# Kernel optimization log

Hardware: AMD Instinct MI355X
Metric: run time of the kernel (lower is better)

## Reference

```python
import jax, jax.numpy as jnp
import numpy as np

NUM_ITERATIONS = 5
DEPTH_L = 2
NUM_NODES = 8448
MAX_CHECK_NEIGHBORS = 10
BATCH = 1024


def setup_inputs() -> dict:
    key = jax.random.key(0)
    k1, k2, k3 = jax.random.split(key, 3)
    input_llr = jax.random.normal(k1, (BATCH, NUM_NODES), dtype=jnp.float32)
    w_ch = jnp.ones((NUM_NODES,), dtype=jnp.float32)
    w_res = jnp.ones((DEPTH_L, NUM_NODES), dtype=jnp.float32)
    check_index_tensor = jax.random.randint(k2, (NUM_NODES, MAX_CHECK_NEIGHBORS), 0, NUM_NODES, dtype=jnp.int32)
    var_index_tensor = jax.random.randint(k3, (NUM_NODES, MAX_CHECK_NEIGHBORS), 0, NUM_NODES, dtype=jnp.int32)
    return {"input_llr": input_llr, "w_ch": w_ch, "w_res": w_res,
            "check_index_tensor": check_index_tensor, "var_index_tensor": var_index_tensor}


def _check_layer(var_messages, check_index_tensor):
    # Gather neighbor variable messages: (B, N, K)
    gathered = var_messages[:, check_index_tensor]
    # tanh-product BP check-node update, numerically clipped
    t = jnp.tanh(jnp.clip(0.5 * gathered, -9.9, 9.9))
    prod = jnp.prod(t, axis=-1)  # (B, N)
    prod = jnp.clip(prod, -0.999999, 0.999999)
    return 2.0 * jnp.arctanh(prod)


def reference(input_llr, w_ch, w_res, check_index_tensor, var_index_tensor):
    weighted_llr = input_llr * w_ch[None, :]
    var_messages = weighted_llr
    prev = []  # deque(maxlen=DEPTH_L), newest first
    for _ in range(NUM_ITERATIONS):
        prev.insert(0, var_messages)
        prev = prev[:DEPTH_L]
        check_messages = _check_layer(var_messages, check_index_tensor)
        residual = sum(w_res[l][None, :] * prev[l] for l in range(len(prev)))
        var_messages = weighted_llr + check_messages + residual
    soft_bits = jax.nn.sigmoid(var_messages + input_llr)
    return soft_bits
```

## Files before the change

### kernel.cpp

```cpp
#include <hip/hip_runtime.h>


#define NN    8448
#define MAXNB 10
#define TPB   1024
#define MAXK  9
#define ITERS 5
#define TBL_BYTES  (NN * 8)
#define LDS_BYTES  (2 * TBL_BYTES)
#define OFFS_INTS  12
#define OFFS_BYTES ((size_t)NN * OFFS_INTS * sizeof(int))
#define WS_NEEDED  OFFS_BYTES

typedef float v2f __attribute__((ext_vector_type(2)));

__global__ __launch_bounds__(256)
void prep_kernel(const int* __restrict__ cidx, const float* __restrict__ w_res,
                 int* __restrict__ offs)
{
    int n = blockIdx.x * 256 + threadIdx.x;
    if (n < NN) {
        #pragma unroll
        for (int j = 0; j < MAXNB; ++j)
            offs[n * OFFS_INTS + j] = cidx[n * MAXNB + j] * 8;
        offs[n * OFFS_INTS + 10] = __float_as_int(w_res[n]);
        offs[n * OFFS_INTS + 11] = __float_as_int(w_res[NN + n]);
    }
}

__device__ __forceinline__ v2f tanh_half(v2f v)
{
    v2f y = __builtin_elementwise_min(
                __builtin_elementwise_max(v, (v2f)(-19.8f)), (v2f)(19.8f));
    v2f e;
    e.x = __expf(y.x);
    e.y = __expf(y.y);
    v2f ab = e + 1.0f;
    float r = __builtin_amdgcn_rcpf(ab.x * ab.y);
    v2f ba = ab.yx;
    v2f inv = ba * r;
    return 1.0f - 2.0f * inv;
}

template<bool USE_OFF>
__global__ __launch_bounds__(TPB)
__attribute__((amdgpu_waves_per_eu(4, 4)))
void ldpc_decode_kernel(const float* __restrict__ input_llr,
                        const float* __restrict__ w_ch,
                        const float* __restrict__ w_res,
                        const int*   __restrict__ cidx,
                        const int*   __restrict__ offs,
                        float* __restrict__ out)
{
    __shared__ __align__(16) char smem[LDS_BYTES];
    const int tid  = threadIdx.x;
    const int row0 = blockIdx.x * 2;
    const float* __restrict__ in0 = input_llr + (size_t)row0 * NN;
    const float* __restrict__ in1 = in0 + NN;
    float* __restrict__ out0 = out + (size_t)row0 * NN;
    float* __restrict__ out1 = out0 + NN;

    v2f wllr[MAXK], vm[MAXK], vmp[MAXK];

    #pragma unroll
    for (int k = 0; k < MAXK; ++k) {
        int n = tid + k * TPB;
        wllr[k] = (v2f)(0.0f);
        vmp[k]  = (v2f)(0.0f);
        if (k < MAXK - 1 || n < NN) {
            float wc = w_ch[n];
            v2f x;
            x.x = in0[n];
            x.y = in1[n];
            wllr[k] = x * wc;
        }
        vm[k] = wllr[k];
        if (k < MAXK - 1 || n < NN) {
            v2f t = tanh_half(vm[k]);
            *(v2f*)(smem + (size_t)n * 8) = t;
        }
    }
    __syncthreads();

    #pragma unroll
    for (int it = 0; it < ITERS; ++it) {
        const int rbase = (it & 1) ? TBL_BYTES : 0;
        const int wbase = (it & 1) ? 0 : TBL_BYTES;
        #pragma unroll
        for (int k = 0; k < MAXK; ++k) {
            int n = tid + k * TPB;
            if (k < MAXK - 1 || n < NN) {
                int o0, o1, o2, o3, o4, o5, o6, o7, o8, o9;
                float wr0, wr1;
                if (USE_OFF) {
                    const int4* op = (const int4*)(offs + n * OFFS_INTS);
                    int4 oA = op[0];
                    int4 oB = op[1];
                    int4 oC = op[2];
                    o0 = oA.x; o1 = oA.y; o2 = oA.z; o3 = oA.w;
                    o4 = oB.x; o5 = oB.y; o6 = oB.z; o7 = oB.w;
                    o8 = oC.x; o9 = oC.y;
                    wr0 = __int_as_float(oC.z);
                    wr1 = __int_as_float(oC.w);
                } else {
                    const int2* ip = (const int2*)(cidx + n * MAXNB);
                    int2 i0 = ip[0], i1 = ip[1], i2 = ip[2], i3 = ip[3], i4 = ip[4];
                    o0 = i0.x << 3; o1 = i0.y << 3;
                    o2 = i1.x << 3; o3 = i1.y << 3;
                    o4 = i2.x << 3; o5 = i2.y << 3;
                    o6 = i3.x << 3; o7 = i3.y << 3;
                    o8 = i4.x << 3; o9 = i4.y << 3;
                    wr0 = w_res[n];
                    wr1 = w_res[NN + n];
                }
                const char* __restrict__ rb = smem + rbase;
                v2f g0 = *(const v2f*)(rb + o0);
                v2f g1 = *(const v2f*)(rb + o1);
                v2f g2 = *(const v2f*)(rb + o2);
                v2f g3 = *(const v2f*)(rb + o3);
                v2f g4 = *(const v2f*)(rb + o4);
                v2f g5 = *(const v2f*)(rb + o5);
                v2f g6 = *(const v2f*)(rb + o6);
                v2f g7 = *(const v2f*)(rb + o7);
                v2f g8 = *(const v2f*)(rb + o8);
                v2f g9 = *(const v2f*)(rb + o9);
                v2f m01 = (g0 * g1) * (g2 * g3);
                v2f m23 = (g4 * g5) * (g6 * g7);
                v2f pr  = (m01 * m23) * (g8 * g9);
                pr = __builtin_elementwise_min(
                         __builtin_elementwise_max(pr, (v2f)(-0.999999f)),
                         (v2f)(0.999999f));
                v2f num = 1.0f + pr;
                v2f den = 1.0f - pr;
                v2f ln, ld;
                ln.x = __log2f(num.x);
                ln.y = __log2f(num.y);
                ld.x = __log2f(den.x);
                ld.y = __log2f(den.y);
                v2f check = (ln - ld) * 0.69314718f;
                v2f res = vm[k] * wr0 + vmp[k] * wr1;
                v2f nv  = (wllr[k] + check) + res;
                vmp[k] = vm[k];
                vm[k]  = nv;
                if (it < ITERS - 1) {
                    v2f t = tanh_half(nv);
                    *(v2f*)(smem + wbase + (size_t)n * 8) = t;
                }
            }
            __builtin_amdgcn_sched_barrier(0);
        }
        if (it < ITERS - 1) __syncthreads();
    }

    #pragma unroll
    for (int k = 0; k < MAXK; ++k) {
        int n = tid + k * TPB;
        if (k < MAXK - 1 || n < NN) {
            float x0 = vm[k].x + in0[n];
            float x1 = vm[k].y + in1[n];
            out0[n] = __fdividef(1.0f, 1.0f + __expf(-x0));
            out1[n] = __fdividef(1.0f, 1.0f + __expf(-x1));
        }
    }
}

extern "C" void kernel_launch(void* const* d_in, const int* in_sizes, int n_in,
                              void* d_out, int out_size, void* d_ws, size_t ws_size,
                              hipStream_t stream) {
    const float* input_llr = (const float*)d_in[0];
    const float* w_ch      = (const float*)d_in[1];
    const float* w_res     = (const float*)d_in[2];
    const int*   cidx      = (const int*)d_in[3];
    float* out = (float*)d_out;
    int batch = in_sizes[0] / NN;
    const bool use_off = (ws_size >= WS_NEEDED) && (d_ws != nullptr);

    if (use_off) {
        int* offs = (int*)d_ws;
        hipLaunchKernelGGL(prep_kernel, dim3((NN + 255) / 256), dim3(256), 0,
                           stream, cidx, w_res, offs);
        hipLaunchKernelGGL(ldpc_decode_kernel<true>, dim3(batch / 2), dim3(TPB),
                           0, stream, input_llr, w_ch, w_res, cidx,
                           offs, out);
    } else {
        hipLaunchKernelGGL(ldpc_decode_kernel<false>, dim3(batch / 2), dim3(TPB),
                           0, stream, input_llr, w_ch, w_res, cidx,
                           nullptr, out);
    }
}
```

Baseline: 152.5 us.

## Store check messages as fp16 log-magnitudes with sign-xor product in LDS

```diff
diff --git a/kernel.cpp b/kernel.cpp
--- a/kernel.cpp
+++ b/kernel.cpp
@@ -1,4 +1,5 @@
 #include <hip/hip_runtime.h>
+#include <hip/hip_fp16.h>
 
 
 #define NN    8448
@@ -6,7 +7,7 @@
 #define TPB   1024
 #define MAXK  9
 #define ITERS 5
-#define TBL_BYTES  (NN * 8)
+#define TBL_BYTES  (NN * 4)
 #define LDS_BYTES  (2 * TBL_BYTES)
 #define OFFS_INTS  12
 #define OFFS_BYTES ((size_t)NN * OFFS_INTS * sizeof(int))
@@ -22,29 +23,29 @@
     if (n < NN) {
         #pragma unroll
         for (int j = 0; j < MAXNB; ++j)
-            offs[n * OFFS_INTS + j] = cidx[n * MAXNB + j] * 8;
+            offs[n * OFFS_INTS + j] = cidx[n * MAXNB + j] * 4;
         offs[n * OFFS_INTS + 10] = __float_as_int(w_res[n]);
         offs[n * OFFS_INTS + 11] = __float_as_int(w_res[NN + n]);
     }
 }
 
-__device__ __forceinline__ v2f tanh_half(v2f v)
+__device__ __forceinline__ unsigned int enc_pair(v2f v)
 {
-    v2f y = __builtin_elementwise_min(
-                __builtin_elementwise_max(v, (v2f)(-19.8f)), (v2f)(19.8f));
-    v2f e;
-    e.x = __expf(y.x);
-    e.y = __expf(y.y);
-    v2f ab = e + 1.0f;
-    float r = __builtin_amdgcn_rcpf(ab.x * ab.y);
-    v2f ba = ab.yx;
-    v2f inv = ba * r;
-    return 1.0f - 2.0f * inv;
+    float z0 = fminf(fabsf(v.x), 19.8f);
+    float z1 = fminf(fabsf(v.y), 19.8f);
+    float u0 = __builtin_amdgcn_exp2f(z0 * -1.44269504f);
+    float u1 = __builtin_amdgcn_exp2f(z1 * -1.44269504f);
+    float m0 = __log2f(1.0f + u0) - __log2f(1.0f - u0);
+    float m1 = __log2f(1.0f + u1) - __log2f(1.0f - u1);
+    m0 = __builtin_copysignf(m0, v.x);
+    m1 = __builtin_copysignf(m1, v.y);
+    unsigned int h0 = __half_as_ushort(__float2half_rn(m0));
+    unsigned int h1 = __half_as_ushort(__float2half_rn(m1));
+    return h0 | (h1 << 16);
 }
 
 template<bool USE_OFF>
 __global__ __launch_bounds__(TPB)
-__attribute__((amdgpu_waves_per_eu(4, 4)))
 void ldpc_decode_kernel(const float* __restrict__ input_llr,
                         const float* __restrict__ w_ch,
                         const float* __restrict__ w_res,
@@ -76,8 +77,7 @@
         }
         vm[k] = wllr[k];
         if (k < MAXK - 1 || n < NN) {
-            v2f t = tanh_half(vm[k]);
-            *(v2f*)(smem + (size_t)n * 8) = t;
+            *(unsigned int*)(smem + (size_t)n * 4) = enc_pair(vm[k]);
         }
     }
     __syncthreads();
@@ -105,46 +105,58 @@
                 } else {
                     const int2* ip = (const int2*)(cidx + n * MAXNB);
                     int2 i0 = ip[0], i1 = ip[1], i2 = ip[2], i3 = ip[3], i4 = ip[4];
-                    o0 = i0.x << 3; o1 = i0.y << 3;
-                    o2 = i1.x << 3; o3 = i1.y << 3;
-                    o4 = i2.x << 3; o5 = i2.y << 3;
-                    o6 = i3.x << 3; o7 = i3.y << 3;
-                    o8 = i4.x << 3; o9 = i4.y << 3;
+                    o0 = i0.x << 2; o1 = i0.y << 2;
+                    o2 = i1.x << 2; o3 = i1.y << 2;
+                    o4 = i2.x << 2; o5 = i2.y << 2;
+                    o6 = i3.x << 2; o7 = i3.y << 2;
+                    o8 = i4.x << 2; o9 = i4.y << 2;
                     wr0 = w_res[n];
                     wr1 = w_res[NN + n];
                 }
                 const char* __restrict__ rb = smem + rbase;
-                v2f g0 = *(const v2f*)(rb + o0);
-                v2f g1 = *(const v2f*)(rb + o1);
-                v2f g2 = *(const v2f*)(rb + o2);
-                v2f g3 = *(const v2f*)(rb + o3);
-                v2f g4 = *(const v2f*)(rb + o4);
-                v2f g5 = *(const v2f*)(rb + o5);
-                v2f g6 = *(const v2f*)(rb + o6);
-                v2f g7 = *(const v2f*)(rb + o7);
-                v2f g8 = *(const v2f*)(rb + o8);
-                v2f g9 = *(const v2f*)(rb + o9);
-                v2f m01 = (g0 * g1) * (g2 * g3);
-                v2f m23 = (g4 * g5) * (g6 * g7);
-                v2f pr  = (m01 * m23) * (g8 * g9);
-                pr = __builtin_elementwise_min(
-                         __builtin_elementwise_max(pr, (v2f)(-0.999999f)),
-                         (v2f)(0.999999f));
-                v2f num = 1.0f + pr;
-                v2f den = 1.0f - pr;
-                v2f ln, ld;
-                ln.x = __log2f(num.x);
-                ln.y = __log2f(num.y);
-                ld.x = __log2f(den.x);
-                ld.y = __log2f(den.y);
-                v2f check = (ln - ld) * 0.69314718f;
+                unsigned int g0 = *(const unsigned int*)(rb + o0);
+                unsigned int g1 = *(const unsigned int*)(rb + o1);
+                unsigned int g2 = *(const unsigned int*)(rb + o2);
+                unsigned int g3 = *(const unsigned int*)(rb + o3);
+                unsigned int g4 = *(const unsigned int*)(rb + o4);
+                unsigned int g5 = *(const unsigned int*)(rb + o5);
+                unsigned int g6 = *(const unsigned int*)(rb + o6);
+                unsigned int g7 = *(const unsigned int*)(rb + o7);
+                unsigned int g8 = *(const unsigned int*)(rb + o8);
+                unsigned int g9 = *(const unsigned int*)(rb + o9);
+                unsigned int xs = ((g0 ^ g1) ^ (g2 ^ g3))
+                                ^ ((g4 ^ g5) ^ (g6 ^ g7)) ^ (g8 ^ g9);
+                #define ABSM(g) ((g) & 0x7fff7fffu)
+                unsigned int a0 = ABSM(g0), a1 = ABSM(g1), a2 = ABSM(g2),
+                             a3 = ABSM(g3), a4 = ABSM(g4), a5 = ABSM(g5),
+                             a6 = ABSM(g6), a7 = ABSM(g7), a8 = ABSM(g8),
+                             a9 = ABSM(g9);
+                #undef ABSM
+                #define LO(a) __half2float(__ushort_as_half((unsigned short)(a)))
+                #define HI(a) __half2float(__ushort_as_half((unsigned short)((a) >> 16)))
+                float L0 = ((LO(a0) + LO(a1)) + (LO(a2) + LO(a3)))
+                         + ((LO(a4) + LO(a5)) + (LO(a6) + LO(a7)))
+                         + (LO(a8) + LO(a9));
+                float L1 = ((HI(a0) + HI(a1)) + (HI(a2) + HI(a3)))
+                         + ((HI(a4) + HI(a5)) + (HI(a6) + HI(a7)))
+                         + (HI(a8) + HI(a9));
+                #undef LO
+                #undef HI
+                float q0 = fminf(__builtin_amdgcn_exp2f(-L0), 0.999999f);
+                float q1 = fminf(__builtin_amdgcn_exp2f(-L1), 0.999999f);
+                float c0 = (__log2f(1.0f + q0) - __log2f(1.0f - q0)) * 0.69314718f;
+                float c1 = (__log2f(1.0f + q1) - __log2f(1.0f - q1)) * 0.69314718f;
+                c0 = __uint_as_float(__float_as_uint(c0) ^ ((xs << 16) & 0x80000000u));
+                c1 = __uint_as_float(__float_as_uint(c1) ^ (xs & 0x80000000u));
+                v2f check;
+                check.x = c0;
+                check.y = c1;
                 v2f res = vm[k] * wr0 + vmp[k] * wr1;
                 v2f nv  = (wllr[k] + check) + res;
                 vmp[k] = vm[k];
                 vm[k]  = nv;
                 if (it < ITERS - 1) {
-                    v2f t = tanh_half(nv);
-                    *(v2f*)(smem + wbase + (size_t)n * 8) = t;
+                    *(unsigned int*)(smem + wbase + (size_t)n * 4) = enc_pair(nv);
                 }
             }
             __builtin_amdgcn_sched_barrier(0);
```

Result: slower. 171.1 us (+12.2%).

## Reorder neighbor indices to balance LDS banks and rematerialize weighted LLR

Applied to the files above, without the earlier changes.

```diff
diff --git a/kernel.cpp b/kernel.cpp
--- a/kernel.cpp
+++ b/kernel.cpp
@@ -6,6 +6,7 @@
 #define TPB   1024
 #define MAXK  9
 #define ITERS 5
+#define NG    (NN / 64)
 #define TBL_BYTES  (NN * 8)
 #define LDS_BYTES  (2 * TBL_BYTES)
 #define OFFS_INTS  12
@@ -14,15 +15,46 @@
 
 typedef float v2f __attribute__((ext_vector_type(2)));
 
-__global__ __launch_bounds__(256)
+__device__ __forceinline__ unsigned getc(unsigned long long c, int b)
+{
+    return (unsigned)(c >> (4 * b)) & 15u;
+}
+
+__global__ __launch_bounds__(64)
 void prep_kernel(const int* __restrict__ cidx, const float* __restrict__ w_res,
                  int* __restrict__ offs)
 {
-    int n = blockIdx.x * 256 + threadIdx.x;
-    if (n < NN) {
-        #pragma unroll
-        for (int j = 0; j < MAXNB; ++j)
-            offs[n * OFFS_INTS + j] = cidx[n * MAXNB + j] * 8;
+    int g = blockIdx.x * 64 + threadIdx.x;
+    if (g >= NG) return;
+    const int base = g * 64;
+    unsigned long long cnt[MAXNB];
+    #pragma unroll
+    for (int j = 0; j < MAXNB; ++j) cnt[j] = 0ull;
+
+    constexpr int PA[3][5] = {{0,1,2,3,4},{0,1,4,5,8},{0,2,4,6,8}};
+    constexpr int PB[3][5] = {{5,6,7,8,9},{2,3,6,7,9},{1,3,5,7,9}};
+
+    for (int r = 0; r < 64; ++r) {
+        int n = base + r;
+        int it[MAXNB];
+        #pragma unroll
+        for (int j = 0; j < MAXNB; ++j) it[j] = cidx[n * MAXNB + j];
+        #pragma unroll
+        for (int rd = 0; rd < 3; ++rd) {
+            #pragma unroll
+            for (int p = 0; p < 5; ++p) {
+                const int a = PA[rd][p], b = PB[rd][p];
+                int ba = it[a] & 15, bb = it[b] & 15;
+                unsigned keep = getc(cnt[a], ba) + getc(cnt[b], bb);
+                unsigned swp  = getc(cnt[a], bb) + getc(cnt[b], ba);
+                if (swp < keep) { int t = it[a]; it[a] = it[b]; it[b] = t; }
+            }
+        }
+        #pragma unroll
+        for (int j = 0; j < MAXNB; ++j) {
+            cnt[j] += 1ull << (4 * (it[j] & 15));
+            offs[n * OFFS_INTS + j] = it[j] * 8;
+        }
         offs[n * OFFS_INTS + 10] = __float_as_int(w_res[n]);
         offs[n * OFFS_INTS + 11] = __float_as_int(w_res[NN + n]);
     }
@@ -44,7 +76,6 @@
 
 template<bool USE_OFF>
 __global__ __launch_bounds__(TPB)
-__attribute__((amdgpu_waves_per_eu(4, 4)))
 void ldpc_decode_kernel(const float* __restrict__ input_llr,
                         const float* __restrict__ w_ch,
                         const float* __restrict__ w_res,
@@ -60,24 +91,20 @@
     float* __restrict__ out0 = out + (size_t)row0 * NN;
     float* __restrict__ out1 = out0 + NN;
 
-    v2f wllr[MAXK], vm[MAXK], vmp[MAXK];
+    v2f vm[MAXK], vmp[MAXK];
 
     #pragma unroll
     for (int k = 0; k < MAXK; ++k) {
         int n = tid + k * TPB;
-        wllr[k] = (v2f)(0.0f);
-        vmp[k]  = (v2f)(0.0f);
+        vmp[k] = (v2f)(0.0f);
+        vm[k]  = (v2f)(0.0f);
         if (k < MAXK - 1 || n < NN) {
             float wc = w_ch[n];
             v2f x;
             x.x = in0[n];
             x.y = in1[n];
-            wllr[k] = x * wc;
-        }
-        vm[k] = wllr[k];
-        if (k < MAXK - 1 || n < NN) {
-            v2f t = tanh_half(vm[k]);
-            *(v2f*)(smem + (size_t)n * 8) = t;
+            vm[k] = x * wc;
+            *(v2f*)(smem + (size_t)n * 8) = tanh_half(vm[k]);
         }
     }
     __syncthreads();
@@ -132,19 +159,19 @@
                          (v2f)(0.999999f));
                 v2f num = 1.0f + pr;
                 v2f den = 1.0f - pr;
-                v2f ln, ld;
-                ln.x = __log2f(num.x);
-                ln.y = __log2f(num.y);
-                ld.x = __log2f(den.x);
-                ld.y = __log2f(den.y);
-                v2f check = (ln - ld) * 0.69314718f;
+                v2f check;
+                check.x = 0.69314718f * (__log2f(num.x) - __log2f(den.x));
+                check.y = 0.69314718f * (__log2f(num.y) - __log2f(den.y));
+                float wc = w_ch[n];
+                v2f x;
+                x.x = in0[n];
+                x.y = in1[n];
                 v2f res = vm[k] * wr0 + vmp[k] * wr1;
-                v2f nv  = (wllr[k] + check) + res;
+                v2f nv  = (x * wc + check) + res;
                 vmp[k] = vm[k];
                 vm[k]  = nv;
                 if (it < ITERS - 1) {
-                    v2f t = tanh_half(nv);
-                    *(v2f*)(smem + wbase + (size_t)n * 8) = t;
+                    *(v2f*)(smem + wbase + (size_t)n * 8) = tanh_half(nv);
                 }
             }
             __builtin_amdgcn_sched_barrier(0);
@@ -177,7 +204,7 @@
 
     if (use_off) {
         int* offs = (int*)d_ws;
-        hipLaunchKernelGGL(prep_kernel, dim3((NN + 255) / 256), dim3(256), 0,
+        hipLaunchKernelGGL(prep_kernel, dim3((NG + 63) / 64), dim3(64), 0,
                            stream, cidx, w_res, offs);
         hipLaunchKernelGGL(ldpc_decode_kernel<true>, dim3(batch / 2), dim3(TPB),
                            0, stream, input_llr, w_ch, w_res, cidx,
```

Measured after the change: 245.7 us. +61.1%, slower.
